# Optimization experiments

Hardware: AMD Instinct MI355X
Metric: run time of the kernel (lower is better)

## Reference

```python
import jax, jax.numpy as jnp
import numpy as np

N_HEAD = 8
D_MODEL = 128  # per-head dim == d_model in this 'interpretable' MHA
B, S = 2, 2048
LN_EPS = 1e-3  # keras LayerNormalization default epsilon


def setup_inputs() -> dict:
    key = jax.random.key(0)
    ks = jax.random.split(key, 8)
    sc = 1.0 / np.sqrt(D_MODEL)
    q = jax.random.normal(ks[0], (B, S, D_MODEL), jnp.float32)
    k = jax.random.normal(ks[1], (B, S, D_MODEL), jnp.float32)
    v = jax.random.normal(ks[2], (B, S, D_MODEL), jnp.float32)
    # multiplicative causal mask (lower-triangular ones), broadcast over B,H
    mask = jnp.tril(jnp.ones((S, S), jnp.float32))[None, None, :, :]
    Wq = jax.random.normal(ks[3], (D_MODEL, N_HEAD * D_MODEL), jnp.float32) * sc
    Wk = jax.random.normal(ks[4], (D_MODEL, N_HEAD * D_MODEL), jnp.float32) * sc
    Wv = jax.random.normal(ks[5], (D_MODEL, N_HEAD * D_MODEL), jnp.float32) * sc
    Wo = jax.random.normal(ks[6], (N_HEAD * D_MODEL, D_MODEL), jnp.float32) * sc
    gamma = jnp.ones((D_MODEL,), jnp.float32)
    beta = jnp.zeros((D_MODEL,), jnp.float32)
    return {"q": q, "k": k, "v": v, "mask": mask, "Wq": Wq, "Wk": Wk,
            "Wv": Wv, "Wo": Wo, "gamma": gamma, "beta": beta}


def reference(q, k, v, mask, Wq, Wk, Wv, Wo, gamma, beta):
    b = q.shape[0]
    # projections -> [B, H, S, D]
    def split_heads(x):
        return x.reshape(b, -1, N_HEAD, D_MODEL).transpose(0, 2, 1, 3)
    qs = split_heads(q @ Wq)
    ks_ = split_heads(k @ Wk)
    vs = split_heads(v @ Wv)
    scores = jnp.einsum('bhqd,bhkd->bhqk', qs, ks_) / jnp.sqrt(jnp.float32(D_MODEL))
    scores = scores * mask  # multiplicative mask (NOT additive -inf)
    attn = jax.nn.softmax(scores, axis=-1)
    # dropout layers are identity at inference
    out = jnp.einsum('bhqk,bhkd->bhqd', attn, vs)
    out = out.transpose(0, 2, 1, 3).reshape(b, -1, N_HEAD * D_MODEL)
    out = out @ Wo
    # keras LayerNorm (axis=-1, eps=1e-3)
    mu = jnp.mean(out, axis=-1, keepdims=True)
    var = jnp.var(out, axis=-1, keepdims=True)
    out = (out - mu) * jax.lax.rsqrt(var + LN_EPS) * gamma + beta
    return out
```

## Files before the change

kernel.cpp:

```cpp
#include <hip/hip_runtime.h>
#include <math.h>

#define B 2
#define S 2048
#define H 8
#define D 128
#define DM 1024
#define BH 16

typedef unsigned short u16;
typedef __attribute__((ext_vector_type(8))) short bf16x8;
typedef __attribute__((ext_vector_type(8))) unsigned short u16x8;
typedef __attribute__((ext_vector_type(4))) float f32x4;

__device__ __forceinline__ float bf2f(u16 x) {
    union { unsigned u; float f; } c; c.u = ((unsigned)x) << 16; return c.f;
}
__device__ __forceinline__ u16 f2bf(float f) {
    union { unsigned u; float f; } c; c.f = f;
    unsigned u = c.u; u += 0x7fffu + ((u >> 16) & 1u);
    return (u16)(u >> 16);
}
__device__ __forceinline__ u16 ftr(float f) {
    union { unsigned u; float f; } c; c.f = f;
    return (u16)(c.u >> 16);
}

#define MFMA16(a, b, c) __builtin_amdgcn_mfma_f32_16x16x32_bf16((a), (b), (c), 0, 0, 0)

__global__ __launch_bounds__(256) void prep_kernel(
    const float* __restrict__ Wq, const float* __restrict__ Wk, const float* __restrict__ Wv,
    const float* __restrict__ Wo, u16* __restrict__ WT, u16* __restrict__ WoT)
{
    __shared__ __align__(16) u16 Wl[128][132];
    int tid = threadIdx.x, by = blockIdx.x;
    if (by < 16) {
        int k0 = by * 64;
#pragma unroll
        for (int i = 0; i < 8; i++) {
            int e = i * 256 + tid; int kk = e >> 5, n4 = e & 31;
            float4 w4 = *(const float4*)&Wo[(size_t)(k0 + kk) * D + n4 * 4];
            ushort4 p; p.x = ftr(w4.x); p.y = ftr(w4.y); p.z = ftr(w4.z); p.w = ftr(w4.w);
            *(ushort4*)&Wl[kk][n4 * 4] = p;
        }
        __syncthreads();
#pragma unroll
        for (int i = 0; i < 4; i++) {
            int e = i * 256 + tid; int n = e >> 3, ko = e & 7;
            u16x8 g;
#pragma unroll
            for (int j = 0; j < 8; j++) g[j] = Wl[ko * 8 + j][n];
            *(u16x8*)&WoT[(size_t)n * DM + k0 + ko * 8] = g;
        }
    } else {
        int tile = by - 16;
        int t = tile >> 3, h = tile & 7;
        const float* W = (t == 0) ? Wq : (t == 1) ? Wk : Wv;
        int col0 = h * 128;
#pragma unroll
        for (int i = 0; i < 16; i++) {
            int e = i * 256 + tid; int kk = e >> 5, n4 = e & 31;
            float4 w4 = *(const float4*)&W[(size_t)kk * DM + col0 + n4 * 4];
            ushort4 p; p.x = ftr(w4.x); p.y = ftr(w4.y); p.z = ftr(w4.z); p.w = ftr(w4.w);
            *(ushort4*)&Wl[kk][n4 * 4] = p;
        }
        __syncthreads();
        u16* WTt = WT + (size_t)tile * (128 * 128);
#pragma unroll
        for (int i = 0; i < 8; i++) {
            int e = i * 256 + tid; int n = e >> 4, ko = e & 15;
            u16x8 g;
#pragma unroll
            for (int j = 0; j < 8; j++) g[j] = Wl[ko * 8 + j][n];
            *(u16x8*)&WTt[(size_t)n * 128 + ko * 8] = g;
        }
    }
}

__global__ __launch_bounds__(256) void proj_kernel(
    const float* __restrict__ q, const float* __restrict__ k, const float* __restrict__ v,
    const u16* __restrict__ WT,
    u16* __restrict__ Qo, u16* __restrict__ Ko, u16* __restrict__ VTo,
    float* __restrict__ Csum)
{
    __shared__ __align__(16) u16 Xs[128][136];
    int tid = threadIdx.x;
    int m0 = blockIdx.x * 128;
    int by = blockIdx.y;
    int t = by >> 3;
    int h = by & 7;
    const float* X = (t == 0) ? q : (t == 1) ? k : v;
    const u16* WTt = WT + (size_t)(t * 8 + h) * (128 * 128);

#pragma unroll
    for (int i = 0; i < 16; i++) {
        int e = i * 256 + tid; int r = e >> 5, c4 = e & 31;
        float4 x4 = *(const float4*)&X[(size_t)(m0 + r) * D + c4 * 4];
        ushort4 p; p.x = ftr(x4.x); p.y = ftr(x4.y); p.z = ftr(x4.z); p.w = ftr(x4.w);
        *(ushort4*)&Xs[r][c4 * 4] = p;
    }
    __syncthreads();

    int w = tid >> 6, lane = tid & 63, quad = lane >> 4, ln = lane & 15;
    bf16x8 aX[2][4];
#pragma unroll
    for (int rf = 0; rf < 2; rf++)
#pragma unroll
        for (int ks = 0; ks < 4; ks++)
            aX[rf][ks] = *(const bf16x8*)&Xs[w * 32 + rf * 16 + ln][ks * 32 + quad * 8];

    f32x4 zero = {0.f, 0.f, 0.f, 0.f};
    f32x4 acc[2][8];
#pragma unroll
    for (int rf = 0; rf < 2; rf++)
#pragma unroll
        for (int nt = 0; nt < 8; nt++) acc[rf][nt] = zero;

#pragma unroll
    for (int ks = 0; ks < 4; ks++) {
        bf16x8 bW[8];
#pragma unroll
        for (int nt = 0; nt < 8; nt++)
            bW[nt] = *(const bf16x8*)&WTt[(size_t)(nt * 16 + ln) * 128 + ks * 32 + quad * 8];
#pragma unroll
        for (int nt = 0; nt < 8; nt++) {
            acc[0][nt] = MFMA16(aX[0][ks], bW[nt], acc[0][nt]);
            acc[1][nt] = MFMA16(aX[1][ks], bW[nt], acc[1][nt]);
        }
    }

    int bb = m0 >> 11, ss0 = m0 & 2047;
    int bh = bb * 8 + h;
    if (t < 2) {
        u16* O = (t == 0) ? Qo : Ko;
#pragma unroll
        for (int rf = 0; rf < 2; rf++)
#pragma unroll
            for (int nt = 0; nt < 8; nt++)
#pragma unroll
                for (int r = 0; r < 4; r++) {
                    int ss = ss0 + w * 32 + rf * 16 + quad * 4 + r;
                    O[((size_t)bh * S + ss) * D + nt * 16 + ln] = f2bf(acc[rf][nt][r]);
                }
    } else {
        __syncthreads();
        u16 (*Ct)[136] = Xs;
#pragma unroll
        for (int rf = 0; rf < 2; rf++)
#pragma unroll
            for (int nt = 0; nt < 8; nt++)
#pragma unroll
                for (int r = 0; r < 4; r++)
                    Ct[nt * 16 + ln][w * 32 + rf * 16 + quad * 4 + r] = f2bf(acc[rf][nt][r]);
        __syncthreads();
#pragma unroll
        for (int i = 0; i < 8; i++) {
            int e = i * 256 + tid; int dloc = e >> 4, s8 = e & 15;
            *(u16x8*)&VTo[((size_t)bh * D + dloc) * S + ss0 + s8 * 8] =
                *(const u16x8*)&Ct[dloc][s8 * 8];
        }
        {
            int d = tid >> 1, c = tid & 1;
            float s = 0.f;
#pragma unroll
            for (int i = 0; i < 8; i++) {
                u16x8 v8 = *(const u16x8*)&Ct[d][c * 64 + i * 8];
#pragma unroll
                for (int j = 0; j < 8; j++) s += bf2f(v8[j]);
            }
            Csum[((size_t)bh * 32 + (ss0 >> 6) + c) * D + d] = s;
        }
    }
}

__global__ __launch_bounds__(128) void scan_kernel(
    const float* __restrict__ Csum, float* __restrict__ SufT)
{
    int bh = blockIdx.x, d = threadIdx.x;
    float acc = 0.f;
    for (int c = 31; c >= 0; c--) {
        SufT[((size_t)bh * 32 + c) * D + d] = acc;
        acc += Csum[((size_t)bh * 32 + c) * D + d];
    }
}

__global__ __launch_bounds__(512, 2) void attn_kernel(
    const u16* __restrict__ Qb, const u16* __restrict__ Kb, const u16* __restrict__ VTg,
    const float* __restrict__ SufT, u16* __restrict__ HOb)
{
    __shared__ __align__(16) u16 Qs[2][64][136];
    __shared__ __align__(16) u16 Ks[128][136];
    __shared__ __align__(16) u16 Vt[128][136];
    __shared__ __align__(16) u16 Ps[2][64][136];
    __shared__ float Lred[2][4][64];

    int tid = threadIdx.x;
    int bx = blockIdx.x, bh = blockIdx.y;
    int nhi = (31 - bx) / 2 + 1, nlo = bx / 2 + 1;
    int w = tid >> 6, qt = w >> 2, wq = w & 3, lane = tid & 63, quad = lane >> 4, ln = lane & 15;
    int qb = qt ? bx : (31 - bx);
    int q0 = qb * 64;
    int nq = qt ? nlo : nhi;
    const u16* Qp  = Qb  + (size_t)bh * S * D;
    const u16* Kp  = Kb  + (size_t)bh * S * D;
    const u16* VTp = VTg + (size_t)bh * D * S;

#pragma unroll
    for (int i = 0; i < 4; i++) {
        int e = i * 512 + tid; int r2 = e >> 4, c8 = e & 15;
        int qtt = r2 >> 6, r = r2 & 63;
        int q0s = (qtt ? bx : (31 - bx)) * 64;
        *(u16x8*)&Qs[qtt][r][c8 * 8] = *(const u16x8*)&Qp[(size_t)(q0s + r) * D + c8 * 8];
    }
    __syncthreads();
    bf16x8 aQ[4][4];
#pragma unroll
    for (int rf = 0; rf < 4; rf++)
#pragma unroll
        for (int ks = 0; ks < 4; ks++)
            aQ[rf][ks] = *(const bf16x8*)&Qs[qt][rf * 16 + ln][ks * 32 + quad * 8];

    f32x4 zero = {0.f, 0.f, 0.f, 0.f};
    f32x4 accPV[4][2], acc_l[4];
#pragma unroll
    for (int rf = 0; rf < 4; rf++) { accPV[rf][0] = zero; accPV[rf][1] = zero; acc_l[rf] = zero; }
    bf16x8 bOnes;
#pragma unroll
    for (int j = 0; j < 8; j++) bOnes[j] = (short)0x3F80;
    const float scale = 0.08838834764831845f;

    for (int kt = 0; kt < nhi; kt++) {
        __syncthreads();
        int k0 = kt * 128;
#pragma unroll
        for (int i = 0; i < 4; i++) {
            int e = i * 512 + tid; int r = e >> 4, c8 = e & 15;
            *(u16x8*)&Ks[r][c8 * 8] = *(const u16x8*)&Kp[(size_t)(k0 + r) * D + c8 * 8];
        }
#pragma unroll
        for (int i = 0; i < 4; i++) {
            int e = i * 512 + tid; int dd = e >> 4, c8 = e & 15;
            *(u16x8*)&Vt[dd][c8 * 8] = *(const u16x8*)&VTp[(size_t)dd * S + k0 + c8 * 8];
        }
        __syncthreads();
        bool active = (qt == 0) || (kt < nlo);
        if (active) {
            f32x4 s[4][2];
#pragma unroll
            for (int rf = 0; rf < 4; rf++) { s[rf][0] = zero; s[rf][1] = zero; }
#pragma unroll
            for (int ks = 0; ks < 4; ks++) {
                bf16x8 b0 = *(const bf16x8*)&Ks[wq * 32 + ln][ks * 32 + quad * 8];
                bf16x8 b1 = *(const bf16x8*)&Ks[wq * 32 + 16 + ln][ks * 32 + quad * 8];
#pragma unroll
                for (int rf = 0; rf < 4; rf++) {
                    s[rf][0] = MFMA16(aQ[rf][ks], b0, s[rf][0]);
                    s[rf][1] = MFMA16(aQ[rf][ks], b1, s[rf][1]);
                }
            }
#pragma unroll
            for (int rf = 0; rf < 4; rf++)
#pragma unroll
                for (int ct = 0; ct < 2; ct++) {
                    int col = k0 + wq * 32 + ct * 16 + ln;
                    int rowb = q0 + rf * 16 + quad * 4;
#pragma unroll
                    for (int r = 0; r < 4; r++) {
                        float tv = (col <= rowb + r) ? s[rf][ct][r] : 0.f;
                        float p = __expf(tv * scale);
                        Ps[qt][rf * 16 + quad * 4 + r][wq * 32 + ct * 16 + ln] = f2bf(p);
                    }
                }
        }
        __syncthreads();
        if (active) {
#pragma unroll
            for (int ks = 0; ks < 4; ks++) {
                bf16x8 aP[4];
#pragma unroll
                for (int rf = 0; rf < 4; rf++)
                    aP[rf] = *(const bf16x8*)&Ps[qt][rf * 16 + ln][ks * 32 + quad * 8];
                bf16x8 v0 = *(const bf16x8*)&Vt[wq * 32 + ln][ks * 32 + quad * 8];
                bf16x8 v1 = *(const bf16x8*)&Vt[wq * 32 + 16 + ln][ks * 32 + quad * 8];
                if (ks == wq) {
#pragma unroll
                    for (int rf = 0; rf < 4; rf++) acc_l[rf] = MFMA16(aP[rf], bOnes, acc_l[rf]);
                }
#pragma unroll
                for (int rf = 0; rf < 4; rf++) {
                    accPV[rf][0] = MFMA16(aP[rf], v0, accPV[rf][0]);
                    accPV[rf][1] = MFMA16(aP[rf], v1, accPV[rf][1]);
                }
            }
        }
    }

    __syncthreads();
    if (ln == 0) {
#pragma unroll
        for (int rf = 0; rf < 4; rf++)
#pragma unroll
            for (int r = 0; r < 4; r++)
                Lred[qt][wq][rf * 16 + quad * 4 + r] = acc_l[rf][r];
    }
    __syncthreads();

    int scount = S - nq * 128;
    size_t sufb = (size_t)(bh * 32 + 2 * nq - 1) * D + wq * 32;
    float suf0 = SufT[sufb + ln];
    float suf1 = SufT[sufb + 16 + ln];
    int b = bh >> 3, h = bh & 7;
#pragma unroll
    for (int rf = 0; rf < 4; rf++)
#pragma unroll
        for (int r = 0; r < 4; r++) {
            int row = rf * 16 + quad * 4 + r;
            int srow = q0 + row;
            float l = Lred[qt][0][row] + Lred[qt][1][row] + Lred[qt][2][row] + Lred[qt][3][row]
                      + (float)scount;
            float inv = 1.f / l;
            size_t base = ((size_t)(b * S + srow)) * DM + h * D + wq * 32;
            HOb[base + ln]      = f2bf((accPV[rf][0][r] + suf0) * inv);
            HOb[base + 16 + ln] = f2bf((accPV[rf][1][r] + suf1) * inv);
        }
}

__global__ __launch_bounds__(256) void out_ln_kernel(
    const u16* __restrict__ HOb, const u16* __restrict__ WoT,
    const float* __restrict__ gamma, const float* __restrict__ beta,
    float* __restrict__ out)
{
    __shared__ __align__(16) u16 HOs[16][1048];
    __shared__ float Cs[16][132];
    int tid = threadIdx.x;
    int m0 = blockIdx.x * 16;
    int w = tid >> 6, lane = tid & 63, quad = lane >> 4, ln = lane & 15;
#pragma unroll
    for (int i = 0; i < 8; i++) {
        int e = i * 256 + tid; int r = e >> 7, c8 = e & 127;
        *(u16x8*)&HOs[r][c8 * 8] = *(const u16x8*)&HOb[(size_t)(m0 + r) * DM + c8 * 8];
    }
    __syncthreads();
    f32x4 zero = {0.f, 0.f, 0.f, 0.f};
    f32x4 acc[2] = {zero, zero};
#pragma unroll 4
    for (int ks = 0; ks < 32; ks++) {
        bf16x8 aH = *(const bf16x8*)&HOs[ln][ks * 32 + quad * 8];
        bf16x8 w0 = *(const bf16x8*)&WoT[(size_t)(w * 32 + ln) * DM + ks * 32 + quad * 8];
        bf16x8 w1 = *(const bf16x8*)&WoT[(size_t)(w * 32 + 16 + ln) * DM + ks * 32 + quad * 8];
        acc[0] = MFMA16(aH, w0, acc[0]);
        acc[1] = MFMA16(aH, w1, acc[1]);
    }
#pragma unroll
    for (int ct = 0; ct < 2; ct++)
#pragma unroll
        for (int r = 0; r < 4; r++)
            Cs[quad * 4 + r][w * 32 + ct * 16 + ln] = acc[ct][r];
    __syncthreads();

    int row = tid >> 4, t16 = tid & 15;
    float xv[8], sum = 0.f, sq = 0.f;
#pragma unroll
    for (int j = 0; j < 8; j++) {
        float x = Cs[row][t16 * 8 + j];
        xv[j] = x; sum += x; sq += x * x;
    }
#pragma unroll
    for (int off = 1; off < 16; off <<= 1) {
        sum += __shfl_xor(sum, off);
        sq  += __shfl_xor(sq, off);
    }
    float mu = sum * (1.f / 128.f);
    float var = sq * (1.f / 128.f) - mu * mu;
    float rstd = rsqrtf(var + 1e-3f);
    float o[8];
#pragma unroll
    for (int j = 0; j < 8; j++) {
        int c = t16 * 8 + j;
        o[j] = (xv[j] - mu) * rstd * gamma[c] + beta[c];
    }
    float* op = &out[(size_t)(m0 + row) * D + t16 * 8];
    *(float4*)&op[0] = *(float4*)&o[0];
    *(float4*)&op[4] = *(float4*)&o[4];
}

extern "C" void kernel_launch(void* const* d_in, const int* in_sizes, int n_in,
                              void* d_out, int out_size, void* d_ws, size_t ws_size,
                              hipStream_t stream)
{
    const float* q     = (const float*)d_in[0];
    const float* k     = (const float*)d_in[1];
    const float* v     = (const float*)d_in[2];
    const float* Wq    = (const float*)d_in[4];
    const float* Wk    = (const float*)d_in[5];
    const float* Wv    = (const float*)d_in[6];
    const float* Wo    = (const float*)d_in[7];
    const float* gamma = (const float*)d_in[8];
    const float* beta  = (const float*)d_in[9];

    u16* ws16 = (u16*)d_ws;
    u16* Qb  = ws16;
    u16* Kb  = ws16 + 4194304;
    u16* VT  = ws16 + 8388608;
    u16* HOb = ws16 + 12582912;
    u16* WoT = ws16 + 16777216;
    u16* WT  = ws16 + 16908288;
    float* Csum = (float*)((char*)d_ws + 35651584);
    float* SufT = (float*)((char*)d_ws + 35913728);

    prep_kernel<<<40, 256, 0, stream>>>(Wq, Wk, Wv, Wo, WT, WoT);
    proj_kernel<<<dim3(32, 24), 256, 0, stream>>>(q, k, v, WT, Qb, Kb, VT, Csum);
    scan_kernel<<<BH, 128, 0, stream>>>(Csum, SufT);
    attn_kernel<<<dim3(16, BH), 512, 0, stream>>>(Qb, Kb, VT, SufT, HOb);
    out_ln_kernel<<<256, 256, 0, stream>>>(HOb, WoT, gamma, beta, (float*)d_out);
}
```

Baseline: 165.4 us.

## Shrink projection tiles, stage weights in LDS, fold suffix scan into attention

The projection kernel now uses 64-row tiles, which doubles the block count, and stages the weight tile in shared memory instead of reading it from global memory per fragment. Q and K outputs are written through an LDS transpose as vectorized rows. The separate scan kernel is removed: each attention block sums the needed chunk totals directly from Csum. The attention grid is also swapped so that heads vary fastest. These changes remove one launch and improve store coalescing, at the cost of a short redundant serial sum inside each attention block.

```diff
diff --git a/kernel.cpp b/kernel.cpp
--- a/kernel.cpp
+++ b/kernel.cpp
@@ -83,9 +83,10 @@
     u16* __restrict__ Qo, u16* __restrict__ Ko, u16* __restrict__ VTo,
     float* __restrict__ Csum)
 {
-    __shared__ __align__(16) u16 Xs[128][136];
+    __shared__ __align__(16) u16 Xs[64][136];
+    __shared__ __align__(16) u16 Ws[128][136];
     int tid = threadIdx.x;
-    int m0 = blockIdx.x * 128;
+    int m0 = blockIdx.x * 64;
     int by = blockIdx.y;
     int t = by >> 3;
     int h = by & 7;
@@ -93,100 +94,89 @@
     const u16* WTt = WT + (size_t)(t * 8 + h) * (128 * 128);
 
 #pragma unroll
-    for (int i = 0; i < 16; i++) {
+    for (int i = 0; i < 8; i++) {
         int e = i * 256 + tid; int r = e >> 5, c4 = e & 31;
         float4 x4 = *(const float4*)&X[(size_t)(m0 + r) * D + c4 * 4];
         ushort4 p; p.x = ftr(x4.x); p.y = ftr(x4.y); p.z = ftr(x4.z); p.w = ftr(x4.w);
         *(ushort4*)&Xs[r][c4 * 4] = p;
     }
+#pragma unroll
+    for (int i = 0; i < 8; i++) {
+        int e = i * 256 + tid; int n = e >> 4, c8 = e & 15;
+        *(u16x8*)&Ws[n][c8 * 8] = *(const u16x8*)&WTt[(size_t)n * 128 + c8 * 8];
+    }
     __syncthreads();
 
     int w = tid >> 6, lane = tid & 63, quad = lane >> 4, ln = lane & 15;
-    bf16x8 aX[2][4];
-#pragma unroll
-    for (int rf = 0; rf < 2; rf++)
-#pragma unroll
-        for (int ks = 0; ks < 4; ks++)
-            aX[rf][ks] = *(const bf16x8*)&Xs[w * 32 + rf * 16 + ln][ks * 32 + quad * 8];
+    bf16x8 aX[4];
+#pragma unroll
+    for (int ks = 0; ks < 4; ks++)
+        aX[ks] = *(const bf16x8*)&Xs[w * 16 + ln][ks * 32 + quad * 8];
 
     f32x4 zero = {0.f, 0.f, 0.f, 0.f};
-    f32x4 acc[2][8];
-#pragma unroll
-    for (int rf = 0; rf < 2; rf++)
-#pragma unroll
-        for (int nt = 0; nt < 8; nt++) acc[rf][nt] = zero;
+    f32x4 acc[8];
+#pragma unroll
+    for (int nt = 0; nt < 8; nt++) acc[nt] = zero;
 
 #pragma unroll
     for (int ks = 0; ks < 4; ks++) {
         bf16x8 bW[8];
 #pragma unroll
         for (int nt = 0; nt < 8; nt++)
-            bW[nt] = *(const bf16x8*)&WTt[(size_t)(nt * 16 + ln) * 128 + ks * 32 + quad * 8];
-#pragma unroll
-        for (int nt = 0; nt < 8; nt++) {
-            acc[0][nt] = MFMA16(aX[0][ks], bW[nt], acc[0][nt]);
-            acc[1][nt] = MFMA16(aX[1][ks], bW[nt], acc[1][nt]);
-        }
+            bW[nt] = *(const bf16x8*)&Ws[nt * 16 + ln][ks * 32 + quad * 8];
+#pragma unroll
+        for (int nt = 0; nt < 8; nt++)
+            acc[nt] = MFMA16(aX[ks], bW[nt], acc[nt]);
     }
 
     int bb = m0 >> 11, ss0 = m0 & 2047;
     int bh = bb * 8 + h;
+    __syncthreads();
     if (t < 2) {
+        u16 (*Ct)[136] = Xs;
         u16* O = (t == 0) ? Qo : Ko;
 #pragma unroll
-        for (int rf = 0; rf < 2; rf++)
-#pragma unroll
-            for (int nt = 0; nt < 8; nt++)
-#pragma unroll
-                for (int r = 0; r < 4; r++) {
-                    int ss = ss0 + w * 32 + rf * 16 + quad * 4 + r;
-                    O[((size_t)bh * S + ss) * D + nt * 16 + ln] = f2bf(acc[rf][nt][r]);
-                }
+        for (int nt = 0; nt < 8; nt++)
+#pragma unroll
+            for (int r = 0; r < 4; r++)
+                Ct[w * 16 + quad * 4 + r][nt * 16 + ln] = f2bf(acc[nt][r]);
+        __syncthreads();
+#pragma unroll
+        for (int i = 0; i < 4; i++) {
+            int e = i * 256 + tid; int r = e >> 4, c8 = e & 15;
+            *(u16x8*)&O[((size_t)bh * S + ss0 + r) * D + c8 * 8] = *(const u16x8*)&Ct[r][c8 * 8];
+        }
     } else {
-        __syncthreads();
-        u16 (*Ct)[136] = Xs;
-#pragma unroll
-        for (int rf = 0; rf < 2; rf++)
-#pragma unroll
-            for (int nt = 0; nt < 8; nt++)
-#pragma unroll
-                for (int r = 0; r < 4; r++)
-                    Ct[nt * 16 + ln][w * 32 + rf * 16 + quad * 4 + r] = f2bf(acc[rf][nt][r]);
-        __syncthreads();
-#pragma unroll
-        for (int i = 0; i < 8; i++) {
-            int e = i * 256 + tid; int dloc = e >> 4, s8 = e & 15;
-            *(u16x8*)&VTo[((size_t)bh * D + dloc) * S + ss0 + s8 * 8] =
-                *(const u16x8*)&Ct[dloc][s8 * 8];
-        }
-        {
-            int d = tid >> 1, c = tid & 1;
+        u16 (*Ct)[68] = (u16 (*)[68])&Xs[0][0];
+#pragma unroll
+        for (int nt = 0; nt < 8; nt++)
+#pragma unroll
+            for (int r = 0; r < 4; r++)
+                Ct[nt * 16 + ln][w * 16 + quad * 4 + r] = f2bf(acc[nt][r]);
+        __syncthreads();
+#pragma unroll
+        for (int i = 0; i < 4; i++) {
+            int e = i * 256 + tid; int dloc = e >> 3, c8 = e & 7;
+            *(u16x8*)&VTo[((size_t)bh * D + dloc) * S + ss0 + c8 * 8] =
+                *(const u16x8*)&Ct[dloc][c8 * 8];
+        }
+        if (tid < 128) {
+            int d = tid;
             float s = 0.f;
 #pragma unroll
             for (int i = 0; i < 8; i++) {
-                u16x8 v8 = *(const u16x8*)&Ct[d][c * 64 + i * 8];
+                u16x8 v8 = *(const u16x8*)&Ct[d][i * 8];
 #pragma unroll
                 for (int j = 0; j < 8; j++) s += bf2f(v8[j]);
             }
-            Csum[((size_t)bh * 32 + (ss0 >> 6) + c) * D + d] = s;
-        }
-    }
-}
-
-__global__ __launch_bounds__(128) void scan_kernel(
-    const float* __restrict__ Csum, float* __restrict__ SufT)
-{
-    int bh = blockIdx.x, d = threadIdx.x;
-    float acc = 0.f;
-    for (int c = 31; c >= 0; c--) {
-        SufT[((size_t)bh * 32 + c) * D + d] = acc;
-        acc += Csum[((size_t)bh * 32 + c) * D + d];
+            Csum[((size_t)bh * 32 + (ss0 >> 6)) * D + d] = s;
+        }
     }
 }
 
 __global__ __launch_bounds__(512, 2) void attn_kernel(
     const u16* __restrict__ Qb, const u16* __restrict__ Kb, const u16* __restrict__ VTg,
-    const float* __restrict__ SufT, u16* __restrict__ HOb)
+    const float* __restrict__ Csum, u16* __restrict__ HOb)
 {
     __shared__ __align__(16) u16 Qs[2][64][136];
     __shared__ __align__(16) u16 Ks[128][136];
@@ -195,7 +185,8 @@
     __shared__ float Lred[2][4][64];
 
     int tid = threadIdx.x;
-    int bx = blockIdx.x, bh = blockIdx.y;
+    int bh = blockIdx.x;
+    int bx = blockIdx.y;
     int nhi = (31 - bx) / 2 + 1, nlo = bx / 2 + 1;
     int w = tid >> 6, qt = w >> 2, wq = w & 3, lane = tid & 63, quad = lane >> 4, ln = lane & 15;
     int qb = qt ? bx : (31 - bx);
@@ -305,10 +296,14 @@
     }
     __syncthreads();
 
+    int nt64 = 2 * nq;
+    float suf0 = 0.f, suf1 = 0.f;
+    for (int c = 31; c >= nt64; c--) {
+        const float* cp = &Csum[((size_t)(bh * 32 + c)) * D + wq * 32];
+        suf0 += cp[ln];
+        suf1 += cp[16 + ln];
+    }
     int scount = S - nq * 128;
-    size_t sufb = (size_t)(bh * 32 + 2 * nq - 1) * D + wq * 32;
-    float suf0 = SufT[sufb + ln];
-    float suf1 = SufT[sufb + 16 + ln];
     int b = bh >> 3, h = bh & 7;
 #pragma unroll
     for (int rf = 0; rf < 4; rf++)
@@ -406,11 +401,9 @@
     u16* WoT = ws16 + 16777216;
     u16* WT  = ws16 + 16908288;
     float* Csum = (float*)((char*)d_ws + 35651584);
-    float* SufT = (float*)((char*)d_ws + 35913728);
 
     prep_kernel<<<40, 256, 0, stream>>>(Wq, Wk, Wv, Wo, WT, WoT);
-    proj_kernel<<<dim3(32, 24), 256, 0, stream>>>(q, k, v, WT, Qb, Kb, VT, Csum);
-    scan_kernel<<<BH, 128, 0, stream>>>(Csum, SufT);
-    attn_kernel<<<dim3(16, BH), 512, 0, stream>>>(Qb, Kb, VT, SufT, HOb);
+    proj_kernel<<<dim3(64, 24), 256, 0, stream>>>(q, k, v, WT, Qb, Kb, VT, Csum);
+    attn_kernel<<<dim3(BH, 16), 512, 0, stream>>>(Qb, Kb, VT, Csum, HOb);
     out_ln_kernel<<<256, 256, 0, stream>>>(HOb, WoT, gamma, beta, (float*)d_out);
 }
```

Measured after the change: 156.8 us, median of 2. 5.2% less time.
